# Optimization experiments

Hardware: AMD Instinct MI355X
Metric: run time of the kernel (lower is better)

The kernel has to match this reference:

```python
import jax, jax.numpy as jnp
import numpy as np

B, SQ, SK, H, NH = 2, 2048, 2048, 1024, 16
HD = H // NH  # 64 per-head dim


def gelu(x):
    # GPT-2 tanh-approx gelu
    return 0.5 * x * (1.0 + jnp.tanh(np.sqrt(2.0 / np.pi) * (x + 0.044715 * x ** 3)))


def setup_inputs() -> dict:
    key = jax.random.key(0)
    ks = jax.random.split(key, 9)
    std = 0.02
    return {
        "attender_seq": jax.random.normal(ks[0], (B, SQ, H), jnp.float32),
        "attendee_seq": jax.random.normal(ks[1], (B, SK, H), jnp.float32),
        "attendee_mask": jax.random.randint(ks[2], (B, SK), 0, 2, jnp.int32),
        "c_attn_w": std * jax.random.normal(ks[3], (H, 3 * H), jnp.float32),
        "c_attn_b": jnp.zeros((3 * H,), jnp.float32),
        "c_proj_w": std * jax.random.normal(ks[4], (H, H), jnp.float32),
        "c_proj_b": jnp.zeros((H,), jnp.float32),
        "mlp_w": std * jax.random.normal(ks[5], (2 * H, H), jnp.float32),
        "mlp_b": jnp.zeros((H,), jnp.float32),
    }


def reference(attender_seq, attendee_seq, attendee_mask,
              c_attn_w, c_attn_b, c_proj_w, c_proj_b, mlp_w, mlp_b):
    # Conv1D == affine: x @ W + b
    qkv_q = attender_seq @ c_attn_w + c_attn_b   # [B,SQ,3H]
    qkv_k = attendee_seq @ c_attn_w + c_attn_b   # [B,SK,3H]
    q = qkv_q[..., :H]
    k = qkv_k[..., H:2 * H]
    v = qkv_k[..., 2 * H:]

    q = q.reshape(B, SQ, NH, HD)
    k = k.reshape(B, SK, NH, HD)
    v = v.reshape(B, SK, NH, HD)

    scores = jnp.einsum('bqhd,bkhd->bhqk', q, k)  # no 1/sqrt(d): scale=False
    # multiplicative (not additive) mask applied post-score, pre-softmax
    scores = scores * attendee_mask.astype(scores.dtype)[:, None, None, :]
    probs = jax.nn.softmax(scores, axis=-1)
    attn = jnp.einsum('bhqk,bkhd->bqhd', probs, v).reshape(B, SQ, H)
    attn = attn @ c_proj_w + c_proj_b            # [B,SQ,H]

    cat = jnp.concatenate([attender_seq, attn], axis=2)  # [B,SQ,2H]
    out = gelu(cat @ mlp_w + mlp_b)              # [B,SQ,H] (dropout = eval identity)
    return out
```

## Files before the change

### kernel.cpp

```cpp
#include <hip/hip_runtime.h>
#include <hip/hip_bf16.h>
#include <math.h>

#define H_ 1024
#define NH_ 16
#define HD_ 64
#define B_ 2
#define SQ_ 2048
#define SK_ 2048

using bf16x8 = __attribute__((ext_vector_type(8))) short;
using f32x4  = __attribute__((ext_vector_type(4))) float;

static __device__ __forceinline__ unsigned short f2bf(float f) {
  union { float f; unsigned u; } v; v.f = f;
  unsigned r = v.u + 0x7fffu + ((v.u >> 16) & 1u);
  return (unsigned short)(r >> 16);
}

static __device__ __forceinline__ unsigned pack_bf(float a, float b) {
  union { float f; unsigned u; } ua, ub;
  ua.f = a; ub.f = b;
  return __builtin_amdgcn_perm(ub.u + 0x8000u, ua.u + 0x8000u, 0x07060302u);
}

static __device__ __forceinline__ void gl2lds16(const void* g, void* l) {
  __builtin_amdgcn_global_load_lds(
      (const __attribute__((address_space(1))) unsigned int*)g,
      (__attribute__((address_space(3))) unsigned int*)l, 16, 0, 0);
}

static __device__ __forceinline__ int sidx(int row, int cbyte) {
  return row * 64 + (((cbyte) ^ ((row & 7) << 4)) >> 1);
}

__global__ __launch_bounds__(256) void conv_bf16(
    const float* __restrict__ src, unsigned short* __restrict__ dst,
    int rows, int cols, int ld_src, int ld_dst) {
  long total = (long)rows * cols / 8;
  for (long i = blockIdx.x * (long)blockDim.x + threadIdx.x; i < total;
       i += (long)gridDim.x * blockDim.x) {
    long e = i * 8;
    int r = (int)(e / cols);
    int c = (int)(e % cols);
    const float* s = src + (long)r * ld_src + c;
    unsigned short tmp[8];
#pragma unroll
    for (int j = 0; j < 8; ++j) tmp[j] = f2bf(s[j]);
    *(uint4*)(dst + (long)r * ld_dst + c) = *(uint4*)tmp;
  }
}

__global__ __launch_bounds__(256) void convT(
    const float* __restrict__ in, unsigned short* __restrict__ out, int R, int C) {
  __shared__ __align__(16) unsigned short Ls[64][68];
  int nct = C >> 6;
  int tr = blockIdx.x / nct, tc = blockIdx.x % nct;
  int r0 = tr * 64, c0 = tc * 64;
  int rr = threadIdx.x >> 4;
  int cc = (threadIdx.x & 15) * 4;
#pragma unroll
  for (int i = 0; i < 4; ++i) {
    int r = rr + 16 * i;
    float4 v = *(const float4*)&in[(long)(r0 + r) * C + c0 + cc];
    unsigned short t[4] = {f2bf(v.x), f2bf(v.y), f2bf(v.z), f2bf(v.w)};
    *(unsigned long long*)&Ls[r][cc] = *(unsigned long long*)t;
  }
  __syncthreads();
  int oc = threadIdx.x >> 2;
  int orr = (threadIdx.x & 3) * 16;
  unsigned short t[16];
#pragma unroll
  for (int j = 0; j < 16; ++j) t[j] = Ls[orr + j][oc];
  *(uint4*)&out[(long)(c0 + oc) * R + r0 + orr] = *(uint4*)&t[0];
  *(uint4*)&out[(long)(c0 + oc) * R + r0 + orr + 8] = *(uint4*)&t[8];
}

template <int NF, int MODE>
__global__ __launch_bounds__(256) void gemm_bt(
    const unsigned short* __restrict__ A, int lda,
    const unsigned short* __restrict__ Bw, int ldb,
    const float* __restrict__ bias, const int* __restrict__ msk,
    void* __restrict__ out0, void* __restrict__ out1, int ldo,
    int M, int N, int K) {
  __shared__ __align__(16) unsigned short Al[2][128 * 64];
  __shared__ __align__(16) unsigned short Bl[2][NF * 32 * 64];
  const int tid = threadIdx.x;
  const int l = tid & 63, w = tid >> 6;
  const int wr = w >> 1, wc = w & 1;
  const int lq = l & 15, lh = l >> 4;
  const int m0 = blockIdx.y * 128, n0 = blockIdx.x * (NF * 32);

  const int swcol = (((tid & 7) ^ ((tid >> 3) & 7)) << 3);
  const int rbase = w * 8 + (l >> 3);
  const unsigned short* gA = A + (long)(m0 + rbase) * lda + swcol;
  const unsigned short* gB = Bw + (long)(n0 + rbase) * ldb + swcol;

  f32x4 acc[4][NF];
#pragma unroll
  for (int a = 0; a < 4; ++a)
#pragma unroll
    for (int b = 0; b < NF; ++b) acc[a][b] = (f32x4){0.f, 0.f, 0.f, 0.f};

  auto stage = [&](int k0, int buf) {
#pragma unroll
    for (int i = 0; i < 4; ++i)
      gl2lds16(gA + (long)(i * 32) * lda + k0, &Al[buf][i * 2048 + w * 512]);
#pragma unroll
    for (int i = 0; i < NF; ++i)
      gl2lds16(gB + (long)(i * 32) * ldb + k0, &Bl[buf][i * 2048 + w * 512]);
  };

  const int NT = K >> 6;
  stage(0, 0);
  __syncthreads();
  int cur = 0;
  for (int t = 0; t < NT; ++t) {
    if (t + 1 < NT) stage((t + 1) << 6, cur ^ 1);
    bf16x8 af[4][2], bfr[NF][2];
#pragma unroll
    for (int a = 0; a < 4; ++a) {
      int row = wr * 64 + a * 16 + lq;
#pragma unroll
      for (int kk = 0; kk < 2; ++kk)
        af[a][kk] = *(const bf16x8*)&Al[cur][sidx(row, kk * 64 + lh * 16)];
    }
#pragma unroll
    for (int b = 0; b < NF; ++b) {
      int row = wc * (NF * 16) + b * 16 + lq;
#pragma unroll
      for (int kk = 0; kk < 2; ++kk)
        bfr[b][kk] = *(const bf16x8*)&Bl[cur][sidx(row, kk * 64 + lh * 16)];
    }
#pragma unroll
    for (int kk = 0; kk < 2; ++kk)
#pragma unroll
      for (int a = 0; a < 4; ++a)
#pragma unroll
        for (int b = 0; b < NF; ++b)
          acc[a][b] = __builtin_amdgcn_mfma_f32_16x16x32_bf16(
              af[a][kk], bfr[b][kk], acc[a][b], 0, 0, 0);
    __syncthreads();
    cur ^= 1;
  }

#pragma unroll
  for (int a = 0; a < 4; ++a) {
#pragma unroll
    for (int bb = 0; bb < NF; ++bb) {
      int col = n0 + wc * (NF * 16) + bb * 16 + lq;
      float bv = bias[col];
      int row0 = m0 + wr * 64 + a * 16 + lh * 4;
      if (MODE == 0) {
        unsigned short* O = (unsigned short*)out0;
#pragma unroll
        for (int r = 0; r < 4; ++r)
          O[(long)(row0 + r) * ldo + col] = f2bf(acc[a][bb][r] + bv);
      } else if (MODE == 1) {
        float* O = (float*)out0;
#pragma unroll
        for (int r = 0; r < 4; ++r) {
          float v = acc[a][bb][r] + bv;
          float y = 0.7978845608028654f * (v + 0.044715f * v * v * v);
          O[(long)(row0 + r) * ldo + col] =
              v * __builtin_amdgcn_rcpf(1.f + __expf(-2.f * y));
        }
      } else {
        if (col < H_) {
          unsigned short* O = (unsigned short*)out0;
#pragma unroll
          for (int r = 0; r < 4; ++r) {
            float mk = (float)msk[row0 + r];
            O[(long)(row0 + r) * ldo + col] = f2bf((acc[a][bb][r] + bv) * mk);
          }
        } else {
          int vcol = col - H_, hh = vcol >> 6, dd = vcol & 63;
          int bi = row0 >> 11, k = row0 & 2047;
          unsigned short t[4];
#pragma unroll
          for (int r = 0; r < 4; ++r) t[r] = f2bf(acc[a][bb][r] + bv);
          *(unsigned long long*)((unsigned short*)out1 +
                                 (((long)(bi * NH_ + hh) * HD_ + dd) << 11) + k) =
              *(unsigned long long*)t;
        }
      }
    }
  }
}

__global__ __launch_bounds__(256) void flash_attn(
    const unsigned short* __restrict__ Qb,
    const unsigned short* __restrict__ Kb,
    const unsigned short* __restrict__ Vtg,
    unsigned short* __restrict__ Ob) {
  __shared__ __align__(16) unsigned short Kl[64 * 64];
  __shared__ __align__(16) unsigned short Vt[64 * 64];
  __shared__ __align__(16) unsigned short Pl[4][1024];
  const int tid = threadIdx.x;
  const int l = tid & 63, w = tid >> 6;
  const int qb = blockIdx.x, h = blockIdx.y, b = blockIdx.z;
  const int lq = l & 15, lh = l >> 4;

  const long qrow = (long)b * SQ_ + qb * 64 + w * 16 + lq;
  const unsigned short* qp = Qb + qrow * H_ + h * HD_;
  const bf16x8 qf0 = *(const bf16x8*)(qp + lh * 8);
  const bf16x8 qf1 = *(const bf16x8*)(qp + 32 + lh * 8);

  const int sr = tid >> 2, scs = (tid & 3) * 16;
  const unsigned short* Kg = Kb + ((long)b * SK_ + sr) * H_ + h * HD_ + scs;
  const unsigned short* Vg = Vtg + ((long)(b * NH_ + h) * HD_ + sr) * SK_ + scs;
  const int wi0 = sidx(sr, (tid & 3) * 32);
  const int wi1 = sidx(sr, (tid & 3) * 32 + 16);

  uint4 kr0 = *(const uint4*)Kg, kr1 = *(const uint4*)(Kg + 8);
  uint4 vr0 = *(const uint4*)Vg, vr1 = *(const uint4*)(Vg + 8);
  *(uint4*)&Kl[wi0] = kr0;
  *(uint4*)&Kl[wi1] = kr1;
  *(uint4*)&Vt[wi0] = vr0;
  *(uint4*)&Vt[wi1] = vr1;

  unsigned short* Pw = Pl[w];
  const float C1 = 1.4426950408889634f;
  const float C2 = 23.083120654223414f;

  float l_run = 0.f;
  f32x4 accO[4];
#pragma unroll
  for (int ms = 0; ms < 4; ++ms) accO[ms] = (f32x4){0.f, 0.f, 0.f, 0.f};

  const int NT = SK_ / 64;
  for (int kt = 0; kt < NT; ++kt) {
    __syncthreads();
    if (kt + 1 < NT) {
      const unsigned short* kp = Kg + (long)(kt + 1) * 64 * H_;
      kr0 = *(const uint4*)kp;
      kr1 = *(const uint4*)(kp + 8);
      vr0 = *(const uint4*)(Vg + (kt + 1) * 64);
      vr1 = *(const uint4*)(Vg + (kt + 1) * 64 + 8);
    }

    f32x4 s[4];
    __builtin_amdgcn_s_setprio(1);
#pragma unroll
    for (int ms = 0; ms < 4; ++ms) {
      int row = ms * 16 + lq;
      bf16x8 a0 = *(const bf16x8*)&Kl[sidx(row, lh * 16)];
      bf16x8 a1 = *(const bf16x8*)&Kl[sidx(row, 64 + lh * 16)];
      f32x4 z = (f32x4){0.f, 0.f, 0.f, 0.f};
      z = __builtin_amdgcn_mfma_f32_16x16x32_bf16(a0, qf0, z, 0, 0, 0);
      z = __builtin_amdgcn_mfma_f32_16x16x32_bf16(a1, qf1, z, 0, 0, 0);
      s[ms] = z;
    }
    __builtin_amdgcn_s_setprio(0);
#pragma unroll
    for (int ms = 0; ms < 4; ++ms) {
      float p0 = exp2f(fmaf(s[ms][0], C1, -C2));
      float p1 = exp2f(fmaf(s[ms][1], C1, -C2));
      float p2 = exp2f(fmaf(s[ms][2], C1, -C2));
      float p3 = exp2f(fmaf(s[ms][3], C1, -C2));
      l_run += (p0 + p1) + (p2 + p3);
      unsigned pk[2] = {pack_bf(p0, p1), pack_bf(p2, p3)};
      *(unsigned long long*)&Pw[sidx(lq, ms * 32 + lh * 8)] =
          *(unsigned long long*)pk;
    }
    bf16x8 pb0 = *(const bf16x8*)&Pw[sidx(lq, lh * 16)];
    bf16x8 pb1 = *(const bf16x8*)&Pw[sidx(lq, 64 + lh * 16)];
    __builtin_amdgcn_s_setprio(1);
#pragma unroll
    for (int ms = 0; ms < 4; ++ms) {
      int row = ms * 16 + lq;
      bf16x8 v0 = *(const bf16x8*)&Vt[sidx(row, lh * 16)];
      bf16x8 v1 = *(const bf16x8*)&Vt[sidx(row, 64 + lh * 16)];
      accO[ms] = __builtin_amdgcn_mfma_f32_16x16x32_bf16(v0, pb0, accO[ms], 0, 0, 0);
      accO[ms] = __builtin_amdgcn_mfma_f32_16x16x32_bf16(v1, pb1, accO[ms], 0, 0, 0);
    }
    __builtin_amdgcn_s_setprio(0);
    __syncthreads();
    if (kt + 1 < NT) {
      *(uint4*)&Kl[wi0] = kr0;
      *(uint4*)&Kl[wi1] = kr1;
      *(uint4*)&Vt[wi0] = vr0;
      *(uint4*)&Vt[wi1] = vr1;
    }
  }

  l_run += __shfl_xor(l_run, 16);
  l_run += __shfl_xor(l_run, 32);
  float rs = 1.f / l_run;
  long orow = (long)b * SQ_ + qb * 64 + w * 16 + lq;
#pragma unroll
  for (int ms = 0; ms < 4; ++ms) {
    unsigned short ou[4];
#pragma unroll
    for (int r = 0; r < 4; ++r) ou[r] = f2bf(accO[ms][r] * rs);
    *(unsigned long long*)(Ob + orow * H_ + h * HD_ + ms * 16 + lh * 4) =
        *(unsigned long long*)ou;
  }
}

extern "C" void kernel_launch(void* const* d_in, const int* in_sizes, int n_in,
                              void* d_out, int out_size, void* d_ws, size_t ws_size,
                              hipStream_t stream) {
  (void)in_sizes; (void)n_in; (void)out_size; (void)ws_size;
  const float* attender = (const float*)d_in[0];
  const float* attendee = (const float*)d_in[1];
  const int*   mask     = (const int*)d_in[2];
  const float* c_attn_w = (const float*)d_in[3];
  const float* c_attn_b = (const float*)d_in[4];
  const float* c_proj_w = (const float*)d_in[5];
  const float* c_proj_b = (const float*)d_in[6];
  const float* mlp_w    = (const float*)d_in[7];
  const float* mlp_b    = (const float*)d_in[8];
  float* out = (float*)d_out;

  char* ws = (char*)d_ws;
  size_t off = 0;
  auto alloc = [&](size_t bytes) {
    void* p = ws + off;
    off += (bytes + 255) & ~(size_t)255;
    return p;
  };
  unsigned short* cat   = (unsigned short*)alloc((size_t)4096 * 2048 * 2);
  unsigned short* aet   = (unsigned short*)alloc((size_t)4096 * 1024 * 2);
  unsigned short* w_atT = (unsigned short*)alloc((size_t)3072 * 1024 * 2);
  unsigned short* w_prT = (unsigned short*)alloc((size_t)1024 * 1024 * 2);
  unsigned short* w_mlT = (unsigned short*)alloc((size_t)1024 * 2048 * 2);
  unsigned short* Qb    = (unsigned short*)alloc((size_t)4096 * 1024 * 2);
  unsigned short* Kbuf  = (unsigned short*)alloc((size_t)4096 * 1024 * 2);
  unsigned short* Vtg   = (unsigned short*)alloc((size_t)B_ * NH_ * HD_ * SK_ * 2);
  unsigned short* attnb = (unsigned short*)alloc((size_t)4096 * 1024 * 2);

  conv_bf16<<<2048, 256, 0, stream>>>(attender, cat, 4096, 1024, 1024, 2048);
  conv_bf16<<<2048, 256, 0, stream>>>(attendee, aet, 4096, 1024, 1024, 1024);
  convT<<<768, 256, 0, stream>>>(c_attn_w, w_atT, 1024, 3072);
  convT<<<256, 256, 0, stream>>>(c_proj_w, w_prT, 1024, 1024);
  convT<<<512, 256, 0, stream>>>(mlp_w, w_mlT, 2048, 1024);

  gemm_bt<2, 0><<<dim3(16, 32), 256, 0, stream>>>(
      cat, 2048, w_atT, 1024, c_attn_b, nullptr, Qb, nullptr, 1024, 4096, 1024, 1024);
  gemm_bt<4, 2><<<dim3(16, 32), 256, 0, stream>>>(
      aet, 1024, w_atT + (size_t)1024 * 1024, 1024, c_attn_b + 1024, mask,
      Kbuf, Vtg, 1024, 4096, 2048, 1024);
  flash_attn<<<dim3(32, 16, 2), 256, 0, stream>>>(Qb, Kbuf, Vtg, attnb);
  gemm_bt<2, 0><<<dim3(16, 32), 256, 0, stream>>>(
      attnb, 1024, w_prT, 1024, c_proj_b, nullptr, cat + 1024, nullptr, 2048, 4096, 1024, 1024);
  gemm_bt<2, 1><<<dim3(16, 32), 256, 0, stream>>>(
      cat, 2048, w_mlT, 2048, mlp_b, nullptr, out, nullptr, 1024, 4096, 1024, 2048);
}
```

Baseline: 186.2 us.

## Fold c_proj into MLP weights, merge QKV GEMMs, write attention into concat buffer

Precomputes a combined weight W_eff = c_proj_w @ mlp_w[H:] and a folded bias, so the separate c_proj GEMM is removed. Flash attention now writes directly into the second half of the concat buffer, and the MLP GEMM reads its second K-half from W_eff. The Q and K/V projections are merged into one launch, and GEMM tiles are widened to 128x128. This trades an extra 1024^3 weight GEMM per call and extra bf16 rounding of the fused weights for one fewer 4096x1024x1024 GEMM and fewer launches.

```diff
diff --git a/kernel.cpp b/kernel.cpp
--- a/kernel.cpp
+++ b/kernel.cpp
@@ -16,6 +16,10 @@
   union { float f; unsigned u; } v; v.f = f;
   unsigned r = v.u + 0x7fffu + ((v.u >> 16) & 1u);
   return (unsigned short)(r >> 16);
+}
+static __device__ __forceinline__ float bf2f(unsigned short u) {
+  union { unsigned u; float f; } c; c.u = (unsigned)u << 16;
+  return c.f;
 }
 
 static __device__ __forceinline__ unsigned pack_bf(float a, float b) {
@@ -76,39 +80,62 @@
   *(uint4*)&out[(long)(c0 + oc) * R + r0 + orr + 8] = *(uint4*)&t[8];
 }
 
-template <int NF, int MODE>
+__global__ __launch_bounds__(256) void bias_fold(
+    const float* __restrict__ mlp_b, const float* __restrict__ cpb,
+    const unsigned short* __restrict__ w_mlT,
+    float* __restrict__ beff) {
+  int wv = threadIdx.x >> 6, l = threadIdx.x & 63;
+  int j = blockIdx.x * 4 + wv;
+  float s = 0.f;
+#pragma unroll
+  for (int i0 = 0; i0 < 1024; i0 += 64)
+    s += cpb[i0 + l] * bf2f(w_mlT[(long)j * 2048 + 1024 + i0 + l]);
+  for (int d = 1; d < 64; d <<= 1) s += __shfl_xor(s, d);
+  if (l == 0) beff[j] = mlp_b[j] + s;
+}
+
+template <int MODE, bool DUALB>
 __global__ __launch_bounds__(256) void gemm_bt(
     const unsigned short* __restrict__ A, int lda,
     const unsigned short* __restrict__ Bw, int ldb,
-    const float* __restrict__ bias, const int* __restrict__ msk,
-    void* __restrict__ out0, void* __restrict__ out1, int ldo,
-    int M, int N, int K) {
+    const unsigned short* __restrict__ Bw2,
+    const float* __restrict__ bias,
+    void* __restrict__ out0, int ldo, int K) {
   __shared__ __align__(16) unsigned short Al[2][128 * 64];
-  __shared__ __align__(16) unsigned short Bl[2][NF * 32 * 64];
+  __shared__ __align__(16) unsigned short Bl[2][128 * 64];
   const int tid = threadIdx.x;
   const int l = tid & 63, w = tid >> 6;
   const int wr = w >> 1, wc = w & 1;
   const int lq = l & 15, lh = l >> 4;
-  const int m0 = blockIdx.y * 128, n0 = blockIdx.x * (NF * 32);
+  const int m0 = blockIdx.y * 128, n0 = blockIdx.x * 128;
 
   const int swcol = (((tid & 7) ^ ((tid >> 3) & 7)) << 3);
   const int rbase = w * 8 + (l >> 3);
   const unsigned short* gA = A + (long)(m0 + rbase) * lda + swcol;
   const unsigned short* gB = Bw + (long)(n0 + rbase) * ldb + swcol;
-
-  f32x4 acc[4][NF];
+  const unsigned short* gB2 =
+      DUALB ? Bw2 + (long)(n0 + rbase) * 1024 + swcol : nullptr;
+
+  f32x4 acc[4][4];
 #pragma unroll
   for (int a = 0; a < 4; ++a)
 #pragma unroll
-    for (int b = 0; b < NF; ++b) acc[a][b] = (f32x4){0.f, 0.f, 0.f, 0.f};
+    for (int b = 0; b < 4; ++b) acc[a][b] = (f32x4){0.f, 0.f, 0.f, 0.f};
 
   auto stage = [&](int k0, int buf) {
 #pragma unroll
     for (int i = 0; i < 4; ++i)
       gl2lds16(gA + (long)(i * 32) * lda + k0, &Al[buf][i * 2048 + w * 512]);
-#pragma unroll
-    for (int i = 0; i < NF; ++i)
-      gl2lds16(gB + (long)(i * 32) * ldb + k0, &Bl[buf][i * 2048 + w * 512]);
+    if (DUALB && k0 >= 1024) {
+#pragma unroll
+      for (int i = 0; i < 4; ++i)
+        gl2lds16(gB2 + (long)(i * 32) * 1024 + (k0 - 1024),
+                 &Bl[buf][i * 2048 + w * 512]);
+    } else {
+#pragma unroll
+      for (int i = 0; i < 4; ++i)
+        gl2lds16(gB + (long)(i * 32) * ldb + k0, &Bl[buf][i * 2048 + w * 512]);
+    }
   };
 
   const int NT = K >> 6;
@@ -117,7 +144,7 @@
   int cur = 0;
   for (int t = 0; t < NT; ++t) {
     if (t + 1 < NT) stage((t + 1) << 6, cur ^ 1);
-    bf16x8 af[4][2], bfr[NF][2];
+    bf16x8 af[4][2], bfr[4][2];
 #pragma unroll
     for (int a = 0; a < 4; ++a) {
       int row = wr * 64 + a * 16 + lq;
@@ -126,8 +153,8 @@
         af[a][kk] = *(const bf16x8*)&Al[cur][sidx(row, kk * 64 + lh * 16)];
     }
 #pragma unroll
-    for (int b = 0; b < NF; ++b) {
-      int row = wc * (NF * 16) + b * 16 + lq;
+    for (int b = 0; b < 4; ++b) {
+      int row = wc * 64 + b * 16 + lq;
 #pragma unroll
       for (int kk = 0; kk < 2; ++kk)
         bfr[b][kk] = *(const bf16x8*)&Bl[cur][sidx(row, kk * 64 + lh * 16)];
@@ -137,7 +164,7 @@
 #pragma unroll
       for (int a = 0; a < 4; ++a)
 #pragma unroll
-        for (int b = 0; b < NF; ++b)
+        for (int b = 0; b < 4; ++b)
           acc[a][b] = __builtin_amdgcn_mfma_f32_16x16x32_bf16(
               af[a][kk], bfr[b][kk], acc[a][b], 0, 0, 0);
     __syncthreads();
@@ -147,8 +174,8 @@
 #pragma unroll
   for (int a = 0; a < 4; ++a) {
 #pragma unroll
-    for (int bb = 0; bb < NF; ++bb) {
-      int col = n0 + wc * (NF * 16) + bb * 16 + lq;
+    for (int bb = 0; bb < 4; ++bb) {
+      int col = n0 + wc * 64 + bb * 16 + lq;
       float bv = bias[col];
       int row0 = m0 + wr * 64 + a * 16 + lh * 4;
       if (MODE == 0) {
@@ -156,7 +183,7 @@
 #pragma unroll
         for (int r = 0; r < 4; ++r)
           O[(long)(row0 + r) * ldo + col] = f2bf(acc[a][bb][r] + bv);
-      } else if (MODE == 1) {
+      } else {
         float* O = (float*)out0;
 #pragma unroll
         for (int r = 0; r < 4; ++r) {
@@ -165,24 +192,110 @@
           O[(long)(row0 + r) * ldo + col] =
               v * __builtin_amdgcn_rcpf(1.f + __expf(-2.f * y));
         }
+      }
+    }
+  }
+}
+
+__global__ __launch_bounds__(256) void gemm_qkv(
+    const unsigned short* __restrict__ Acat,
+    const unsigned short* __restrict__ Aet,
+    const unsigned short* __restrict__ Bw,
+    const float* __restrict__ bias,
+    const int* __restrict__ msk,
+    unsigned short* __restrict__ Qb,
+    unsigned short* __restrict__ Kb,
+    unsigned short* __restrict__ Vtg) {
+  __shared__ __align__(16) unsigned short Al[2][128 * 64];
+  __shared__ __align__(16) unsigned short Bl[2][128 * 64];
+  const int tid = threadIdx.x;
+  const int l = tid & 63, w = tid >> 6;
+  const int wr = w >> 1, wc = w & 1;
+  const int lq = l & 15, lh = l >> 4;
+  const int bx = blockIdx.x;
+  const int m0 = blockIdx.y * 128, n0 = bx * 128;
+  const unsigned short* A;
+  int lda;
+  if (bx < 8) { A = Acat; lda = 2048; } else { A = Aet; lda = 1024; }
+
+  const int swcol = (((tid & 7) ^ ((tid >> 3) & 7)) << 3);
+  const int rbase = w * 8 + (l >> 3);
+  const unsigned short* gA = A + (long)(m0 + rbase) * lda + swcol;
+  const unsigned short* gB = Bw + (long)(n0 + rbase) * 1024 + swcol;
+
+  f32x4 acc[4][4];
+#pragma unroll
+  for (int a = 0; a < 4; ++a)
+#pragma unroll
+    for (int b = 0; b < 4; ++b) acc[a][b] = (f32x4){0.f, 0.f, 0.f, 0.f};
+
+  auto stage = [&](int k0, int buf) {
+#pragma unroll
+    for (int i = 0; i < 4; ++i)
+      gl2lds16(gA + (long)(i * 32) * lda + k0, &Al[buf][i * 2048 + w * 512]);
+#pragma unroll
+    for (int i = 0; i < 4; ++i)
+      gl2lds16(gB + (long)(i * 32) * 1024 + k0, &Bl[buf][i * 2048 + w * 512]);
+  };
+
+  stage(0, 0);
+  __syncthreads();
+  int cur = 0;
+  for (int t = 0; t < 16; ++t) {
+    if (t + 1 < 16) stage((t + 1) << 6, cur ^ 1);
+    bf16x8 af[4][2], bfr[4][2];
+#pragma unroll
+    for (int a = 0; a < 4; ++a) {
+      int row = wr * 64 + a * 16 + lq;
+#pragma unroll
+      for (int kk = 0; kk < 2; ++kk)
+        af[a][kk] = *(const bf16x8*)&Al[cur][sidx(row, kk * 64 + lh * 16)];
+    }
+#pragma unroll
+    for (int b = 0; b < 4; ++b) {
+      int row = wc * 64 + b * 16 + lq;
+#pragma unroll
+      for (int kk = 0; kk < 2; ++kk)
+        bfr[b][kk] = *(const bf16x8*)&Bl[cur][sidx(row, kk * 64 + lh * 16)];
+    }
+#pragma unroll
+    for (int kk = 0; kk < 2; ++kk)
+#pragma unroll
+      for (int a = 0; a < 4; ++a)
+#pragma unroll
+        for (int b = 0; b < 4; ++b)
+          acc[a][b] = __builtin_amdgcn_mfma_f32_16x16x32_bf16(
+              af[a][kk], bfr[b][kk], acc[a][b], 0, 0, 0);
+    __syncthreads();
+    cur ^= 1;
+  }
+
+#pragma unroll
+  for (int a = 0; a < 4; ++a) {
+#pragma unroll
+    for (int bb = 0; bb < 4; ++bb) {
+      int col = n0 + wc * 64 + bb * 16 + lq;
+      float bv = bias[col];
+      int row0 = m0 + wr * 64 + a * 16 + lh * 4;
+      if (col < 1024) {
+#pragma unroll
+        for (int r = 0; r < 4; ++r)
+          Qb[(long)(row0 + r) * 1024 + col] = f2bf(acc[a][bb][r] + bv);
+      } else if (col < 2048) {
+        int kcol = col - 1024;
+#pragma unroll
+        for (int r = 0; r < 4; ++r) {
+          float mk = (float)msk[row0 + r];
+          Kb[(long)(row0 + r) * 1024 + kcol] = f2bf((acc[a][bb][r] + bv) * mk);
+        }
       } else {
-        if (col < H_) {
-          unsigned short* O = (unsigned short*)out0;
-#pragma unroll
-          for (int r = 0; r < 4; ++r) {
-            float mk = (float)msk[row0 + r];
-            O[(long)(row0 + r) * ldo + col] = f2bf((acc[a][bb][r] + bv) * mk);
-          }
-        } else {
-          int vcol = col - H_, hh = vcol >> 6, dd = vcol & 63;
-          int bi = row0 >> 11, k = row0 & 2047;
-          unsigned short t[4];
-#pragma unroll
-          for (int r = 0; r < 4; ++r) t[r] = f2bf(acc[a][bb][r] + bv);
-          *(unsigned long long*)((unsigned short*)out1 +
-                                 (((long)(bi * NH_ + hh) * HD_ + dd) << 11) + k) =
-              *(unsigned long long*)t;
-        }
+        int vcol = col - 2048, hh = vcol >> 6, dd = vcol & 63;
+        int bi = row0 >> 11, k = row0 & 2047;
+        unsigned short t[4];
+#pragma unroll
+        for (int r = 0; r < 4; ++r) t[r] = f2bf(acc[a][bb][r] + bv);
+        *(unsigned long long*)(Vtg + (((long)(bi * NH_ + hh) * HD_ + dd) << 11) + k) =
+            *(unsigned long long*)t;
       }
     }
   }
@@ -192,7 +305,7 @@
     const unsigned short* __restrict__ Qb,
     const unsigned short* __restrict__ Kb,
     const unsigned short* __restrict__ Vtg,
-    unsigned short* __restrict__ Ob) {
+    unsigned short* __restrict__ Ob, int ldo) {
   __shared__ __align__(16) unsigned short Kl[64 * 64];
   __shared__ __align__(16) unsigned short Vt[64 * 64];
   __shared__ __align__(16) unsigned short Pl[4][1024];
@@ -293,7 +406,7 @@
     unsigned short ou[4];
 #pragma unroll
     for (int r = 0; r < 4; ++r) ou[r] = f2bf(accO[ms][r] * rs);
-    *(unsigned long long*)(Ob + orow * H_ + h * HD_ + ms * 16 + lh * 4) =
+    *(unsigned long long*)(Ob + orow * ldo + h * HD_ + ms * 16 + lh * 4) =
         *(unsigned long long*)ou;
   }
 }
@@ -323,27 +436,28 @@
   unsigned short* cat   = (unsigned short*)alloc((size_t)4096 * 2048 * 2);
   unsigned short* aet   = (unsigned short*)alloc((size_t)4096 * 1024 * 2);
   unsigned short* w_atT = (unsigned short*)alloc((size_t)3072 * 1024 * 2);
-  unsigned short* w_prT = (unsigned short*)alloc((size_t)1024 * 1024 * 2);
+  unsigned short* w_pr  = (unsigned short*)alloc((size_t)1024 * 1024 * 2);
   unsigned short* w_mlT = (unsigned short*)alloc((size_t)1024 * 2048 * 2);
+  unsigned short* weffT = (unsigned short*)alloc((size_t)1024 * 1024 * 2);
   unsigned short* Qb    = (unsigned short*)alloc((size_t)4096 * 1024 * 2);
   unsigned short* Kbuf  = (unsigned short*)alloc((size_t)4096 * 1024 * 2);
   unsigned short* Vtg   = (unsigned short*)alloc((size_t)B_ * NH_ * HD_ * SK_ * 2);
-  unsigned short* attnb = (unsigned short*)alloc((size_t)4096 * 1024 * 2);
-
+  float* beff = (float*)alloc(1024 * 4);
+  float* zbuf = (float*)alloc(1024 * 4);
+
+  hipMemsetAsync(zbuf, 0, 1024 * 4, stream);
   conv_bf16<<<2048, 256, 0, stream>>>(attender, cat, 4096, 1024, 1024, 2048);
   conv_bf16<<<2048, 256, 0, stream>>>(attendee, aet, 4096, 1024, 1024, 1024);
   convT<<<768, 256, 0, stream>>>(c_attn_w, w_atT, 1024, 3072);
-  convT<<<256, 256, 0, stream>>>(c_proj_w, w_prT, 1024, 1024);
+  conv_bf16<<<512, 256, 0, stream>>>(c_proj_w, w_pr, 1024, 1024, 1024, 1024);
   convT<<<512, 256, 0, stream>>>(mlp_w, w_mlT, 2048, 1024);
 
-  gemm_bt<2, 0><<<dim3(16, 32), 256, 0, stream>>>(
-      cat, 2048, w_atT, 1024, c_attn_b, nullptr, Qb, nullptr, 1024, 4096, 1024, 1024);
-  gemm_bt<4, 2><<<dim3(16, 32), 256, 0, stream>>>(
-      aet, 1024, w_atT + (size_t)1024 * 1024, 1024, c_attn_b + 1024, mask,
-      Kbuf, Vtg, 1024, 4096, 2048, 1024);
-  flash_attn<<<dim3(32, 16, 2), 256, 0, stream>>>(Qb, Kbuf, Vtg, attnb);
-  gemm_bt<2, 0><<<dim3(16, 32), 256, 0, stream>>>(
-      attnb, 1024, w_prT, 1024, c_proj_b, nullptr, cat + 1024, nullptr, 2048, 4096, 1024, 1024);
-  gemm_bt<2, 1><<<dim3(16, 32), 256, 0, stream>>>(
-      cat, 2048, w_mlT, 2048, mlp_b, nullptr, out, nullptr, 1024, 4096, 1024, 2048);
-}
+  bias_fold<<<256, 256, 0, stream>>>(mlp_b, c_proj_b, w_mlT, beff);
+  gemm_bt<0, false><<<dim3(8, 8), 256, 0, stream>>>(
+      w_mlT + 1024, 2048, w_pr, 1024, nullptr, zbuf, weffT, 1024, 1024);
+  gemm_qkv<<<dim3(24, 32), 256, 0, stream>>>(
+      cat, aet, w_atT, c_attn_b, mask, Qb, Kbuf, Vtg);
+  flash_attn<<<dim3(32, 16, 2), 256, 0, stream>>>(Qb, Kbuf, Vtg, cat + 1024, 2048);
+  gemm_bt<1, true><<<dim3(8, 32), 256, 0, stream>>>(
+      cat, 2048, w_mlT, 2048, weffT, beff, out, 1024, 2048);
+}
```

Result: slower. 216.9 us (+16.5%).
